# Kernel tuning notes

Hardware: AMD Instinct MI355X
Metric: run time of the kernel (lower is better)

## Reference

```python
import jax, jax.numpy as jnp
import numpy as np

DIM = 512
NSLOTS = 8
ITERS = 3
EPS = 1e-8
LN_EPS = 1e-5
SCALE = DIM ** -0.5


def _ln(x, g, b):
    m = jnp.mean(x, axis=-1, keepdims=True)
    v = jnp.mean((x - m) ** 2, axis=-1, keepdims=True)
    return (x - m) / jnp.sqrt(v + LN_EPS) * g + b


def _gru(x, h, W_ih, W_hh, b_ih, b_hh):
    # PyTorch GRUCell, gate order r,z,n
    gi = x @ W_ih.T + b_ih
    gh = h @ W_hh.T + b_hh
    ir, iz, inn = jnp.split(gi, 3, axis=-1)
    hr, hz, hn = jnp.split(gh, 3, axis=-1)
    r = jax.nn.sigmoid(ir + hr)
    z = jax.nn.sigmoid(iz + hz)
    n = jnp.tanh(inn + r * hn)
    return (1.0 - z) * n + z * h


def _norm_attn(dots):
    # softmax over slot axis, then renormalize over token axis
    a = jax.nn.softmax(dots, axis=1)
    return a / (jnp.sum(a, axis=-1, keepdims=True) + EPS)


def setup_inputs() -> dict:
    key = jax.random.key(0)
    ks = jax.random.split(key, 16)
    b, na, ni = 32, 1024, 3136
    d, hd = DIM, DIM  # hidden_dim = max(dim, 128) = 512
    s = 0.02
    inp = {
        'inputs_audio': jax.random.normal(ks[0], (b, na, d), jnp.float32),
        'inputs_image': jax.random.normal(ks[1], (b, ni, d), jnp.float32),
        'slots_noise': jax.random.normal(ks[2], (b, NSLOTS, d), jnp.float32),
        'slots_mu': jax.random.normal(ks[3], (1, 1, d), jnp.float32),
        'slots_logsigma': jnp.zeros((1, 1, d), jnp.float32),
        'ln_in_g': jnp.ones((d,), jnp.float32), 'ln_in_b': jnp.zeros((d,), jnp.float32),
        'ln_slots_g': jnp.ones((d,), jnp.float32), 'ln_slots_b': jnp.zeros((d,), jnp.float32),
        'ln_ff_g': jnp.ones((d,), jnp.float32), 'ln_ff_b': jnp.zeros((d,), jnp.float32),
        'Wq': jax.random.normal(ks[4], (d, d), jnp.float32) * s, 'bq': jnp.zeros((d,), jnp.float32),
        'Wk': jax.random.normal(ks[5], (d, d), jnp.float32) * s, 'bk': jnp.zeros((d,), jnp.float32),
        'Wv': jax.random.normal(ks[6], (d, d), jnp.float32) * s, 'bv': jnp.zeros((d,), jnp.float32),
        'W_ih': jax.random.normal(ks[7], (3 * d, d), jnp.float32) * s,
        'W_hh': jax.random.normal(ks[8], (3 * d, d), jnp.float32) * s,
        'b_ih': jnp.zeros((3 * d,), jnp.float32), 'b_hh': jnp.zeros((3 * d,), jnp.float32),
        'W1': jax.random.normal(ks[9], (hd, d), jnp.float32) * s, 'b1': jnp.zeros((hd,), jnp.float32),
        'W2': jax.random.normal(ks[10], (d, hd), jnp.float32) * s, 'b2': jnp.zeros((d,), jnp.float32),
    }
    return inp


def reference(inputs_audio, inputs_image, slots_noise, slots_mu, slots_logsigma,
              ln_in_g, ln_in_b, ln_slots_g, ln_slots_b, ln_ff_g, ln_ff_b,
              Wq, bq, Wk, bk, Wv, bv, W_ih, W_hh, b_ih, b_hh, W1, b1, W2, b2):
    b, na, d = inputs_audio.shape
    slots0 = slots_mu + jnp.exp(slots_logsigma) * slots_noise  # [b, S, d]

    ia = _ln(inputs_audio, ln_in_g, ln_in_b)
    ii = _ln(inputs_image, ln_in_g, ln_in_b)
    k_a = ia @ Wk.T + bk
    v_a = ia @ Wv.T + bv
    k_i = ii @ Wk.T + bk
    v_i = ii @ Wv.T + bv

    def mlp(x):
        return jax.nn.relu(x @ W1.T + b1) @ W2.T + b2

    def step(slots, k, v):
        prev = slots
        sn = _ln(slots, ln_slots_g, ln_slots_b)
        q = sn @ Wq.T + bq
        dots = jnp.einsum('bid,bjd->bij', q, k) * SCALE
        attn = _norm_attn(dots)
        upd = jnp.einsum('bjd,bij->bid', v, attn)
        h = _gru(upd.reshape(-1, d), prev.reshape(-1, d), W_ih, W_hh, b_ih, b_hh)
        slots = h.reshape(b, -1, d)
        slots = slots + mlp(_ln(slots, ln_ff_g, ln_ff_b))
        return slots, q, attn

    slots_a, slots_i = slots0, slots0
    for _ in range(ITERS):
        slots_a, q_a, attn_a = step(slots_a, k_a, v_a)
        slots_i, q_i, attn_i = step(slots_i, k_i, v_i)

    cross_ai = _norm_attn(jnp.einsum('bid,bjd->bij', q_a, k_i) * SCALE)  # audio->image
    cross_ia = _norm_attn(jnp.einsum('bid,bjd->bij', q_i, k_a) * SCALE)  # image->audio

    return (slots_a, q_a, k_a, attn_a, cross_ia,
            slots_i, q_i, k_i, attn_i, cross_ai)
```

## Files before the change

### kernel.cpp

```cpp
#include <hip/hip_runtime.h>
#include <hip/hip_bf16.h>

#define DIM 512
#define EPS 1e-8f
#define LN_EPS 1e-5f
#define SCALE 0.04419417382415922f

typedef float f32x4 __attribute__((ext_vector_type(4)));
typedef __bf16 bf16;
typedef __bf16 bf16x8 __attribute__((ext_vector_type(8)));

typedef const __attribute__((address_space(1))) void gvoid;
typedef __attribute__((address_space(3))) void lvoid;

__device__ inline float bf2f_lo(unsigned u) { union { unsigned x; float f; } c; c.x = u << 16; return c.f; }
__device__ inline float bf2f_hi(unsigned u) { union { unsigned x; float f; } c; c.x = u & 0xffff0000u; return c.f; }

#define SBAR() do { __builtin_amdgcn_sched_barrier(0); \
                    __builtin_amdgcn_s_barrier(); \
                    __builtin_amdgcn_sched_barrier(0); } while (0)

__global__ __launch_bounds__(256) void k_stats_convert(
    const float* __restrict__ x, bf16* __restrict__ xbf,
    float* __restrict__ stats, int M)
{
  int row = blockIdx.x * 4 + (threadIdx.x >> 6);
  int lane = threadIdx.x & 63;
  if (row >= M) return;
  const float* xr = x + (size_t)row * DIM;
  float4 a = *(const float4*)(xr + lane * 8);
  float4 b = *(const float4*)(xr + lane * 8 + 4);
  float s  = a.x + a.y + a.z + a.w + b.x + b.y + b.z + b.w;
  float ss = a.x*a.x + a.y*a.y + a.z*a.z + a.w*a.w
           + b.x*b.x + b.y*b.y + b.z*b.z + b.w*b.w;
  for (int off = 32; off; off >>= 1) { s += __shfl_xor(s, off); ss += __shfl_xor(ss, off); }
  float mean = s * (1.0f / DIM);
  float var  = ss * (1.0f / DIM) - mean * mean;
  float rs   = rsqrtf(var + LN_EPS);
  if (lane == 0) { stats[row * 2] = mean; stats[row * 2 + 1] = rs; }
  union { bf16 h[8]; uint4 u; } cv;
  cv.h[0] = (bf16)a.x; cv.h[1] = (bf16)a.y; cv.h[2] = (bf16)a.z; cv.h[3] = (bf16)a.w;
  cv.h[4] = (bf16)b.x; cv.h[5] = (bf16)b.y; cv.h[6] = (bf16)b.z; cv.h[7] = (bf16)b.w;
  *(uint4*)(xbf + (size_t)row * DIM + lane * 8) = cv.u;
}

__global__ __launch_bounds__(256) void k_stats512(
    const float* __restrict__ x, float* __restrict__ stats)
{
  int row = blockIdx.x * 4 + (threadIdx.x >> 6);
  int lane = threadIdx.x & 63;
  const float* xr = x + (size_t)row * DIM;
  float4 a = *(const float4*)(xr + lane * 8);
  float4 b = *(const float4*)(xr + lane * 8 + 4);
  float s  = a.x + a.y + a.z + a.w + b.x + b.y + b.z + b.w;
  float ss = a.x*a.x + a.y*a.y + a.z*a.z + a.w*a.w
           + b.x*b.x + b.y*b.y + b.z*b.z + b.w*b.w;
  for (int off = 32; off; off >>= 1) { s += __shfl_xor(s, off); ss += __shfl_xor(ss, off); }
  float mean = s * (1.0f / DIM);
  float rs   = rsqrtf(ss * (1.0f / DIM) - mean * mean + LN_EPS);
  if (lane == 0) { stats[row * 2] = mean; stats[row * 2 + 1] = rs; }
}

__global__ __launch_bounds__(64) void k_prep(
    const float* __restrict__ Wk, const float* __restrict__ bk,
    const float* __restrict__ Wv, const float* __restrict__ bv,
    const float* __restrict__ g_in, const float* __restrict__ b_in,
    const float* __restrict__ Wq, const float* __restrict__ bq,
    const float* __restrict__ g_s, const float* __restrict__ b_s,
    const float* __restrict__ W1, const float* __restrict__ b1,
    const float* __restrict__ g_f, const float* __restrict__ b_f,
    bf16* __restrict__ wbf, float* __restrict__ c1kv, float* __restrict__ c2kv,
    float* __restrict__ Wqp, float* __restrict__ cq1, float* __restrict__ cq2,
    float* __restrict__ W1p, float* __restrict__ cf1, float* __restrict__ cf2)
{
  int n = blockIdx.x; int lane = threadIdx.x;
  if (n < 1024) {
    const float* W = (n < DIM) ? (Wk + (size_t)n * DIM) : (Wv + (size_t)(n - DIM) * DIM);
    float bias = (n < DIM) ? bk[n] : bv[n - DIM];
    float s1 = 0.f, s2 = 0.f;
    union { bf16 h[8]; uint4 u; } cv;
#pragma unroll
    for (int j = 0; j < 8; ++j) {
      int d = lane * 8 + j;
      float w = W[d];
      float gw = g_in[d] * w;
      s1 += gw; s2 += b_in[d] * w;
      cv.h[j] = (bf16)gw;
    }
    *(uint4*)(wbf + (size_t)n * DIM + lane * 8) = cv.u;
    for (int off = 32; off; off >>= 1) { s1 += __shfl_xor(s1, off); s2 += __shfl_xor(s2, off); }
    if (lane == 0) { c1kv[n] = s1; c2kv[n] = s2 + bias; }
  } else {
    int m; const float* W; float bias; const float* g; const float* b;
    float* Wp; float* cc1; float* cc2;
    if (n < 1536) { m = n - 1024; W = Wq + (size_t)m * DIM; bias = bq[m]; g = g_s; b = b_s; Wp = Wqp; cc1 = cq1; cc2 = cq2; }
    else          { m = n - 1536; W = W1 + (size_t)m * DIM; bias = b1[m]; g = g_f; b = b_f; Wp = W1p; cc1 = cf1; cc2 = cf2; }
    float s1 = 0.f, s2 = 0.f;
    float arr[8];
#pragma unroll
    for (int j = 0; j < 8; ++j) {
      int d = lane * 8 + j;
      float w = W[d];
      float gw = g[d] * w;
      s1 += gw; s2 += b[d] * w;
      arr[j] = gw;
    }
    *(float4*)(Wp + (size_t)m * DIM + lane * 8)     = make_float4(arr[0], arr[1], arr[2], arr[3]);
    *(float4*)(Wp + (size_t)m * DIM + lane * 8 + 4) = make_float4(arr[4], arr[5], arr[6], arr[7]);
    for (int off = 32; off; off >>= 1) { s1 += __shfl_xor(s1, off); s2 += __shfl_xor(s2, off); }
    if (lane == 0) { cc1[m] = s1; cc2[m] = s2 + bias; }
  }
}

__global__ __launch_bounds__(256, 4) void k_kv_gemm(
    const bf16* __restrict__ xa, const bf16* __restrict__ xi,
    const bf16* __restrict__ wbf,
    const float* __restrict__ sa, const float* __restrict__ si,
    const float* __restrict__ c1, const float* __restrict__ c2,
    float* __restrict__ ka, float* __restrict__ ki,
    bf16* __restrict__ kba, bf16* __restrict__ kbi,
    bf16* __restrict__ va, bf16* __restrict__ vi,
    int nblkA, int nblkTot)
{
  __shared__ bf16 As[2][128 * 32];
  __shared__ bf16 Bs[2][128 * 32];
  const int t = threadIdx.x, wave = t >> 6, lane = t & 63;
  int bid = blockIdx.x;
  int rid = (bid & 7) * (nblkTot >> 3) + (bid >> 3);
  bool isA = rid < nblkA;
  int lrid = isA ? rid : rid - nblkA;
  const bf16* x = isA ? xa : xi;
  const float* stats = isA ? sa : si;
  float* kout = isA ? ka : ki;
  bf16* kbf = isA ? kba : kbi;
  bf16* vbf = isA ? va : vi;
  const int row0 = (lrid >> 3) * 128, col0 = (lrid & 7) * 128;
  f32x4 acc[4][4] = {};

  const int sr  = wave * 16 + (lane >> 2);
  const int sgl = ((lane & 3) ^ ((lane >> 3) & 3)) * 8;
  const bf16* asrc = x   + (size_t)(row0 + sr) * DIM + sgl;
  const bf16* bsrc = wbf + (size_t)(col0 + sr) * DIM + sgl;

  auto stage = [&](int buf, int k0) {
#pragma unroll
    for (int p = 0; p < 2; ++p) {
      __builtin_amdgcn_global_load_lds(
          (gvoid*)(asrc + (size_t)(p * 64) * DIM + k0),
          (lvoid*)((char*)&As[buf][0] + (p * 256 + wave * 64) * 16), 16, 0, 0);
      __builtin_amdgcn_global_load_lds(
          (gvoid*)(bsrc + (size_t)(p * 64) * DIM + k0),
          (lvoid*)((char*)&Bs[buf][0] + (p * 256 + wave * 64) * 16), 16, 0, 0);
    }
  };

  const int l15 = lane & 15, q16 = lane >> 4;
  const int wm = wave >> 1, wn = wave & 1;
  const int gpx = (q16 ^ ((l15 >> 1) & 3)) * 8;

  stage(0, 0);
  stage(1, 32);
  asm volatile("s_waitcnt vmcnt(4)" ::: "memory");
  SBAR();
  int cur = 0;
  for (int ks = 0; ks < 16; ++ks) {
    const bf16* Ab = &As[cur][0];
    const bf16* Bb = &Bs[cur][0];
    bf16x8 ax[4], bw[4];
#pragma unroll
    for (int mi = 0; mi < 4; ++mi)
      ax[mi] = *(const bf16x8*)(Ab + (wm * 64 + mi * 16 + l15) * 32 + gpx);
#pragma unroll
    for (int ni = 0; ni < 4; ++ni)
      bw[ni] = *(const bf16x8*)(Bb + (wn * 64 + ni * 16 + l15) * 32 + gpx);
#pragma unroll
    for (int ni = 0; ni < 4; ++ni)
#pragma unroll
      for (int mi = 0; mi < 4; ++mi)
        acc[ni][mi] = __builtin_amdgcn_mfma_f32_16x16x32_bf16(bw[ni], ax[mi], acc[ni][mi], 0, 0, 0);
    SBAR();
    if (ks < 14) {
      stage(cur, (ks + 2) * 32);
      asm volatile("s_waitcnt vmcnt(4)" ::: "memory");
      SBAR();
    } else if (ks == 14) {
      asm volatile("s_waitcnt vmcnt(0)" ::: "memory");
      SBAR();
    }
    cur ^= 1;
  }

#pragma unroll
  for (int mi = 0; mi < 4; ++mi) {
    int row = row0 + wm * 64 + mi * 16 + l15;
    float2 st = *(const float2*)&stats[row * 2];
    float rs = st.y, rm = st.y * st.x;
#pragma unroll
    for (int ni = 0; ni < 4; ++ni) {
      int col = col0 + wn * 64 + ni * 16 + q16 * 4;
      float4 c1v = *(const float4*)&c1[col];
      float4 c2v = *(const float4*)&c2[col];
      f32x4 a = acc[ni][mi];
      float4 o;
      o.x = rs * a[0] - rm * c1v.x + c2v.x;
      o.y = rs * a[1] - rm * c1v.y + c2v.y;
      o.z = rs * a[2] - rm * c1v.z + c2v.z;
      o.w = rs * a[3] - rm * c1v.w + c2v.w;
      union { bf16 h[4]; uint2 u; } pk;
      pk.h[0] = (bf16)o.x; pk.h[1] = (bf16)o.y; pk.h[2] = (bf16)o.z; pk.h[3] = (bf16)o.w;
      if (col0 < DIM) {
        *(float4*)&kout[(size_t)row * DIM + col] = o;
        if (kbf) *(uint2*)&kbf[(size_t)row * DIM + col] = pk.u;
      } else {
        *(uint2*)&vbf[(size_t)row * DIM + (col - DIM)] = pk.u;
      }
    }
  }
}

__global__ __launch_bounds__(256) void k_f2bf(
    const float* __restrict__ in, bf16* __restrict__ out)
{
  size_t i = ((size_t)blockIdx.x * 256 + threadIdx.x) * 8;
  float4 a = *(const float4*)(in + i);
  float4 b = *(const float4*)(in + i + 4);
  union { bf16 h[8]; uint4 u; } cv;
  cv.h[0] = (bf16)a.x; cv.h[1] = (bf16)a.y; cv.h[2] = (bf16)a.z; cv.h[3] = (bf16)a.w;
  cv.h[4] = (bf16)b.x; cv.h[5] = (bf16)b.y; cv.h[6] = (bf16)b.z; cv.h[7] = (bf16)b.w;
  *(uint4*)(out + i) = cv.u;
}

__global__ __launch_bounds__(256) void k_init_slots(
    const float* __restrict__ noise, const float* __restrict__ mu,
    const float* __restrict__ lsig, float* __restrict__ slots)
{
  int idx = blockIdx.x * 256 + threadIdx.x;
  int d = idx & (DIM - 1);
  float v = mu[d] + expf(lsig[d]) * noise[idx];
  slots[idx] = v;
  slots[131072 + idx] = v;
}

template <int MODE>
__global__ __launch_bounds__(128) void k_sgemm(
    const float* __restrict__ A, const float* __restrict__ B, int N,
    float* __restrict__ C,
    const float* __restrict__ c1a, const float* __restrict__ c2a,
    const float* __restrict__ stats,
    const float* __restrict__ bias, const float* __restrict__ invden,
    const float* __restrict__ R,
    float* __restrict__ outA, float* __restrict__ outI,
    bf16* __restrict__ qbf)
{
  __shared__ float As[32][33];
  __shared__ float Bs[64][33];
  int t = threadIdx.x;
  int m0 = blockIdx.y * 32, n0 = blockIdx.x * 64;
  float acc[4][4] = {};
  for (int k0 = 0; k0 < DIM; k0 += 32) {
    __syncthreads();
#pragma unroll
    for (int p = 0; p < 2; ++p) {
      int idx = p * 128 + t, r = idx >> 3, c4 = (idx & 7) * 4;
      float4 v = *(const float4*)(A + (size_t)(m0 + r) * DIM + k0 + c4);
      As[r][c4] = v.x; As[r][c4 + 1] = v.y; As[r][c4 + 2] = v.z; As[r][c4 + 3] = v.w;
    }
#pragma unroll
    for (int p = 0; p < 4; ++p) {
      int idx = p * 128 + t, r = idx >> 3, c4 = (idx & 7) * 4;
      float4 v = *(const float4*)(B + (size_t)(n0 + r) * DIM + k0 + c4);
      Bs[r][c4] = v.x; Bs[r][c4 + 1] = v.y; Bs[r][c4 + 2] = v.z; Bs[r][c4 + 3] = v.w;
    }
    __syncthreads();
    int tr = t >> 4, tc = t & 15;
#pragma unroll
    for (int k = 0; k < 32; ++k) {
      float a0 = As[tr * 4][k], a1 = As[tr * 4 + 1][k], a2 = As[tr * 4 + 2][k], a3 = As[tr * 4 + 3][k];
      float b0 = Bs[tc * 4][k], b1 = Bs[tc * 4 + 1][k], b2 = Bs[tc * 4 + 2][k], b3 = Bs[tc * 4 + 3][k];
      acc[0][0] += a0 * b0; acc[0][1] += a0 * b1; acc[0][2] += a0 * b2; acc[0][3] += a0 * b3;
      acc[1][0] += a1 * b0; acc[1][1] += a1 * b1; acc[1][2] += a1 * b2; acc[1][3] += a1 * b3;
      acc[2][0] += a2 * b0; acc[2][1] += a2 * b1; acc[2][2] += a2 * b2; acc[2][3] += a2 * b3;
      acc[3][0] += a3 * b0; acc[3][1] += a3 * b1; acc[3][2] += a3 * b2; acc[3][3] += a3 * b3;
    }
  }
  int tr = t >> 4, tc = t & 15;
#pragma unroll
  for (int mi = 0; mi < 4; ++mi) {
    int row = m0 + tr * 4 + mi;
#pragma unroll
    for (int ni = 0; ni < 4; ++ni) {
      int col = n0 + tc * 4 + ni;
      float v = acc[mi][ni];
      if (MODE == 0 || MODE == 3) {
        float mean = stats[row * 2], rs = stats[row * 2 + 1];
        v = rs * v - rs * mean * c1a[col] + c2a[col];
      }
      if (MODE == 4) v += bias[col];
      if (MODE == 3) v = fmaxf(v, 0.0f);
      if (MODE == 4) v += R[(size_t)row * N + col];
      if (MODE == 0) {
        if (row < 256) outA[(size_t)row * DIM + col] = v;
        else           outI[(size_t)(row - 256) * DIM + col] = v;
        qbf[(size_t)row * DIM + col] = (bf16)(v * SCALE);
      } else {
        C[(size_t)row * N + col] = v;
        if (MODE == 4 && outA) {
          if (row < 256) outA[(size_t)row * DIM + col] = v;
          else           outI[(size_t)(row - 256) * DIM + col] = v;
        }
      }
    }
  }
}

__global__ __launch_bounds__(128) void k_gates(
    const float* __restrict__ num, const float* __restrict__ slots,
    const float* __restrict__ Wih, const float* __restrict__ Whh,
    const float* __restrict__ bih, const float* __restrict__ bhh,
    const float* __restrict__ invden,
    float* __restrict__ gib, float* __restrict__ ghb)
{
  bool first = blockIdx.x < 24;
  const float* A = first ? num : slots;
  const float* B = first ? Wih : Whh;
  const float* bias = first ? bih : bhh;
  float* C = first ? gib : ghb;
  int n0 = (first ? blockIdx.x : blockIdx.x - 24) * 64;
  int m0 = blockIdx.y * 32;
  __shared__ float As[32][33];
  __shared__ float Bs[64][33];
  int t = threadIdx.x;
  float acc[4][4] = {};
  for (int k0 = 0; k0 < DIM; k0 += 32) {
    __syncthreads();
#pragma unroll
    for (int p = 0; p < 2; ++p) {
      int idx = p * 128 + t, r = idx >> 3, c4 = (idx & 7) * 4;
      float4 v = *(const float4*)(A + (size_t)(m0 + r) * DIM + k0 + c4);
      As[r][c4] = v.x; As[r][c4 + 1] = v.y; As[r][c4 + 2] = v.z; As[r][c4 + 3] = v.w;
    }
#pragma unroll
    for (int p = 0; p < 4; ++p) {
      int idx = p * 128 + t, r = idx >> 3, c4 = (idx & 7) * 4;
      float4 v = *(const float4*)(B + (size_t)(n0 + r) * DIM + k0 + c4);
      Bs[r][c4] = v.x; Bs[r][c4 + 1] = v.y; Bs[r][c4 + 2] = v.z; Bs[r][c4 + 3] = v.w;
    }
    __syncthreads();
    int tr = t >> 4, tc = t & 15;
#pragma unroll
    for (int k = 0; k < 32; ++k) {
      float a0 = As[tr * 4][k], a1 = As[tr * 4 + 1][k], a2 = As[tr * 4 + 2][k], a3 = As[tr * 4 + 3][k];
      float b0 = Bs[tc * 4][k], b1 = Bs[tc * 4 + 1][k], b2 = Bs[tc * 4 + 2][k], b3 = Bs[tc * 4 + 3][k];
      acc[0][0] += a0 * b0; acc[0][1] += a0 * b1; acc[0][2] += a0 * b2; acc[0][3] += a0 * b3;
      acc[1][0] += a1 * b0; acc[1][1] += a1 * b1; acc[1][2] += a1 * b2; acc[1][3] += a1 * b3;
      acc[2][0] += a2 * b0; acc[2][1] += a2 * b1; acc[2][2] += a2 * b2; acc[2][3] += a2 * b3;
      acc[3][0] += a3 * b0; acc[3][1] += a3 * b1; acc[3][2] += a3 * b2; acc[3][3] += a3 * b3;
    }
  }
  int tr = t >> 4, tc = t & 15;
#pragma unroll
  for (int mi = 0; mi < 4; ++mi) {
    int row = m0 + tr * 4 + mi;
    float sc = first ? invden[row] : 1.0f;
#pragma unroll
    for (int ni = 0; ni < 4; ++ni) {
      int col = n0 + tc * 4 + ni;
      C[(size_t)row * 1536 + col] = acc[mi][ni] * sc + bias[col];
    }
  }
}

__global__ __launch_bounds__(256) void k_dots(
    const bf16* __restrict__ qA, const bf16* __restrict__ qI,
    const bf16* __restrict__ kA, const bf16* __restrict__ kI,
    float* __restrict__ aoutA, float* __restrict__ aoutI,
    float* __restrict__ denp, int NA_, int NI_)
{
  __shared__ bf16 ks[2][128 * 64];
  __shared__ float dsh[32];
  int t = threadIdx.x, wave = t >> 6, lane = t & 63;
  int b = blockIdx.y, tile = blockIdx.x;
  bool isA = tile < 8;
  int til = isA ? tile : tile - 8;
  int N = isA ? NA_ : NI_;
  int j0 = til * 128;
  const bf16* q = (isA ? qA : qI) + (size_t)b * 8 * DIM;
  const bf16* k = (isA ? kA : kI) + (size_t)b * N * DIM;
  float* aout = (isA ? aoutA : aoutI) + (size_t)b * 8 * N;
  int drow = (isA ? 0 : 256) + b * 8;

  const int l15 = lane & 15, q16 = lane >> 4;
  bf16x8 afq[16];
  {
    const bf16* qr = q + (size_t)(l15 & 7) * DIM + q16 * 8;
#pragma unroll
    for (int f = 0; f < 16; ++f)
      afq[f] = *(const bf16x8*)(qr + f * 32);
  }

  const int sr  = wave * 8 + (lane >> 3);
  const int sgl = ((lane & 7) ^ (lane >> 3)) * 8;
  int jr = j0 + sr; if (jr > N - 1) jr = N - 1;
  const bf16* ksrc = k + (size_t)jr * DIM + sgl;
  int jr2 = j0 + 32 + sr; if (jr2 > N - 1) jr2 = N - 1;
  const bf16* ksrc2 = k + (size_t)jr2 * DIM + sgl;
  int jr3 = j0 + 64 + sr; if (jr3 > N - 1) jr3 = N - 1;
  const bf16* ksrc3 = k + (size_t)jr3 * DIM + sgl;
  int jr4 = j0 + 96 + sr; if (jr4 > N - 1) jr4 = N - 1;
  const bf16* ksrc4 = k + (size_t)jr4 * DIM + sgl;

  auto stage = [&](int buf, int c) {
    __builtin_amdgcn_global_load_lds((gvoid*)(ksrc  + c * 64),
        (lvoid*)((char*)&ks[buf][0] + (0 * 256 + wave * 64) * 16), 16, 0, 0);
    __builtin_amdgcn_global_load_lds((gvoid*)(ksrc2 + c * 64),
        (lvoid*)((char*)&ks[buf][0] + (1 * 256 + wave * 64) * 16), 16, 0, 0);
    __builtin_amdgcn_global_load_lds((gvoid*)(ksrc3 + c * 64),
        (lvoid*)((char*)&ks[buf][0] + (2 * 256 + wave * 64) * 16), 16, 0, 0);
    __builtin_amdgcn_global_load_lds((gvoid*)(ksrc4 + c * 64),
        (lvoid*)((char*)&ks[buf][0] + (3 * 256 + wave * 64) * 16), 16, 0, 0);
  };

  stage(0, 0);
  stage(1, 1);
  asm volatile("s_waitcnt vmcnt(4)" ::: "memory");
  SBAR();
  f32x4 acc[2] = {};
  int cur = 0;
  for (int c = 0; c < 8; ++c) {
#pragma unroll
    for (int kk = 0; kk < 2; ++kk) {
#pragma unroll
      for (int n = 0; n < 2; ++n) {
        int R = wave * 32 + n * 16 + l15;
        int gp = (kk * 4 + q16) ^ (R & 7);
        bf16x8 bfr = *(const bf16x8*)(&ks[cur][0] + R * 64 + gp * 8);
        acc[n] = __builtin_amdgcn_mfma_f32_16x16x32_bf16(afq[c * 2 + kk], bfr, acc[n], 0, 0, 0);
      }
    }
    SBAR();
    if (c < 6) {
      stage(cur, c + 2);
      asm volatile("s_waitcnt vmcnt(4)" ::: "memory");
      SBAR();
    } else if (c == 6) {
      asm volatile("s_waitcnt vmcnt(0)" ::: "memory");
      SBAR();
    }
    cur ^= 1;
  }

  float dsum[8];
#pragma unroll
  for (int i = 0; i < 8; ++i) dsum[i] = 0.f;
#pragma unroll
  for (int n = 0; n < 2; ++n) {
    int j = j0 + wave * 32 + n * 16 + l15;
    float dv[8];
#pragma unroll
    for (int r = 0; r < 4; ++r) {
      float own = acc[n][r];
      float oth = __shfl_xor(own, 16);
      if (q16 == 0) { dv[r] = own; dv[4 + r] = oth; }
      else          { dv[r] = oth; dv[4 + r] = own; }
    }
    float mx = dv[0];
#pragma unroll
    for (int i = 1; i < 8; ++i) mx = fmaxf(mx, dv[i]);
    float sum = 0.f;
#pragma unroll
    for (int i = 0; i < 8; ++i) { dv[i] = __expf(dv[i] - mx); sum += dv[i]; }
    float inv = 1.0f / sum;
    bool valid = (j < N);
#pragma unroll
    for (int i = 0; i < 8; ++i) {
      float av = valid ? dv[i] * inv : 0.0f;
      dsum[i] += av;
      if (valid && q16 == 0) aout[(size_t)i * N + j] = av;
    }
  }
#pragma unroll
  for (int i = 0; i < 8; ++i) {
    float v = dsum[i];
    v += __shfl_xor(v, 1); v += __shfl_xor(v, 2);
    v += __shfl_xor(v, 4); v += __shfl_xor(v, 8);
    dsum[i] = v;
  }
  if (lane == 0) {
#pragma unroll
    for (int i = 0; i < 8; ++i) dsh[wave * 8 + i] = dsum[i];
  }
  __syncthreads();
  if (t < 8) {
    float den = dsh[t] + dsh[8 + t] + dsh[16 + t] + dsh[24 + t];
    denp[((size_t)drow + t) * 32 + til] = den;
  }
}

__global__ __launch_bounds__(256) void k_upd(
    const bf16* __restrict__ vA, const bf16* __restrict__ vI,
    const float* __restrict__ aA, const float* __restrict__ aI,
    float* __restrict__ numpA, float* __restrict__ numpI, int NA_, int NI_)
{
  __shared__ float ash[128 * 12];
  int t = threadIdx.x, b = blockIdx.y, x = blockIdx.x;
  bool isA = x < 4;
  int c = isA ? x : x - 4;
  int N = isA ? NA_ : NI_;
  int nc = isA ? 4 : 13;
  int jstart = c * 256;
  int jend = jstart + 256; if (jend > N) jend = N;
  const bf16* v = (isA ? vA : vI) + (size_t)b * N * DIM;
  const float* a = (isA ? aA : aI) + (size_t)b * 8 * N;
  float acc[16] = {};
  int d0 = t * 2;
  for (int jt = jstart; jt < jend; jt += 128) {
    int jmax = jend - jt; if (jmax > 128) jmax = 128;
    __syncthreads();
    {
      int i = t >> 5, jq = (t & 31) * 4;
      float4 av = make_float4(0.f, 0.f, 0.f, 0.f);
      if (jt + jq < N) av = *(const float4*)&a[(size_t)i * N + jt + jq];
      ash[(jq + 0) * 12 + i] = av.x;
      ash[(jq + 1) * 12 + i] = av.y;
      ash[(jq + 2) * 12 + i] = av.z;
      ash[(jq + 3) * 12 + i] = av.w;
    }
    __syncthreads();
    for (int jj = 0; jj < jmax; ++jj) {
      unsigned vv = *(const unsigned*)(v + (size_t)(jt + jj) * DIM + d0);
      float v0 = bf2f_lo(vv), v1 = bf2f_hi(vv);
      float4 a0 = *(const float4*)&ash[jj * 12];
      float4 a1 = *(const float4*)&ash[jj * 12 + 4];
      acc[0]  += a0.x * v0; acc[1]  += a0.x * v1;
      acc[2]  += a0.y * v0; acc[3]  += a0.y * v1;
      acc[4]  += a0.z * v0; acc[5]  += a0.z * v1;
      acc[6]  += a0.w * v0; acc[7]  += a0.w * v1;
      acc[8]  += a1.x * v0; acc[9]  += a1.x * v1;
      acc[10] += a1.y * v0; acc[11] += a1.y * v1;
      acc[12] += a1.z * v0; acc[13] += a1.z * v1;
      acc[14] += a1.w * v0; acc[15] += a1.w * v1;
    }
  }
  float* np = (isA ? numpA : numpI) + (((size_t)b * nc + c) * 8) * DIM;
#pragma unroll
  for (int i = 0; i < 8; ++i)
    *(float2*)&np[(size_t)i * DIM + d0] = make_float2(acc[i * 2], acc[i * 2 + 1]);
}

__global__ __launch_bounds__(256) void k_numred(
    const float* __restrict__ numpA, const float* __restrict__ numpI,
    const float* __restrict__ denp,
    float* __restrict__ num, float* __restrict__ invden)
{
  int m = blockIdx.x, t = threadIdx.x;
  bool isA = m < 256;
  int mm = isA ? m : m - 256;
  int bb = mm >> 3, i = mm & 7;
  int nc = isA ? 4 : 13;
  const float* np = (isA ? numpA : numpI) + (((size_t)bb * nc) * 8 + i) * DIM;
  int d0 = t * 2;
  float s0 = 0.f, s1 = 0.f;
  for (int c = 0; c < nc; ++c) {
    float2 vv = *(const float2*)&np[(size_t)c * 8 * DIM + d0];
    s0 += vv.x; s1 += vv.y;
  }
  *(float2*)&num[(size_t)m * DIM + d0] = make_float2(s0, s1);
  if (t == 0) {
    int nch = isA ? 8 : 25;
    float den = EPS;
    for (int c2 = 0; c2 < nch; ++c2) den += denp[(size_t)m * 32 + c2];
    invden[m] = 1.0f / den;
  }
}

__global__ __launch_bounds__(256) void k_gru(
    const float* __restrict__ gi, const float* __restrict__ gh,
    const float* __restrict__ prev,
    float* __restrict__ hout, float* __restrict__ stats_h)
{
  int m = blockIdx.x; int t = threadIdx.x;
  size_t b3 = (size_t)m * 1536, b1 = (size_t)m * DIM;
  float h[2]; float s = 0.f, ss = 0.f;
#pragma unroll
  for (int p = 0; p < 2; ++p) {
    int d = t + p * 256;
    float ir = gi[b3 + d], iz = gi[b3 + 512 + d], in_ = gi[b3 + 1024 + d];
    float hr = gh[b3 + d], hz = gh[b3 + 512 + d], hn = gh[b3 + 1024 + d];
    float r = 1.f / (1.f + __expf(-(ir + hr)));
    float z = 1.f / (1.f + __expf(-(iz + hz)));
    float n = tanhf(in_ + r * hn);
    float hv = (1.f - z) * n + z * prev[b1 + d];
    hout[b1 + d] = hv;
    h[p] = hv; s += hv; ss += hv * hv;
  }
  for (int off = 32; off; off >>= 1) { s += __shfl_xor(s, off); ss += __shfl_xor(ss, off); }
  __shared__ float red[8];
  int wv = t >> 6, ln = t & 63;
  if (ln == 0) { red[wv] = s; red[4 + wv] = ss; }
  __syncthreads();
  s = red[0] + red[1] + red[2] + red[3];
  ss = red[4] + red[5] + red[6] + red[7];
  float mean = s * (1.0f / DIM);
  float rs = rsqrtf(ss * (1.0f / DIM) - mean * mean + LN_EPS);
  if (t == 0) { stats_h[m * 2] = mean; stats_h[m * 2 + 1] = rs; }
}

__global__ __launch_bounds__(256) void k_renorm2(
    const float* __restrict__ aA, const float* __restrict__ aI,
    const float* __restrict__ denp,
    float* __restrict__ outA, float* __restrict__ outI, int NA_, int NI_)
{
  int m = blockIdx.x; int t = threadIdx.x;
  bool isA = m < 256;
  int mm = isA ? m : m - 256;
  int N = isA ? NA_ : NI_;
  int nch = isA ? 8 : 25;
  const float* in = (isA ? aA : aI) + (size_t)mm * N;
  float* out = (isA ? outA : outI) + (size_t)mm * N;
  float den = EPS;
  for (int c = 0; c < nch; ++c) den += denp[(size_t)m * 32 + c];
  float inv = 1.0f / den;
  for (int idx = t; idx * 4 < N; idx += 256) {
    float4 v = *(const float4*)&in[idx * 4];
    v.x *= inv; v.y *= inv; v.z *= inv; v.w *= inv;
    *(float4*)&out[idx * 4] = v;
  }
}

extern "C" void kernel_launch(void* const* d_in, const int* in_sizes, int n_in,
                              void* d_out, int out_size, void* d_ws, size_t ws_size,
                              hipStream_t stream)
{
  (void)in_sizes; (void)n_in; (void)out_size;
  const float* x_a   = (const float*)d_in[0];
  const float* x_i   = (const float*)d_in[1];
  const float* noise = (const float*)d_in[2];
  const float* mu    = (const float*)d_in[3];
  const float* lsig  = (const float*)d_in[4];
  const float* ln_in_g = (const float*)d_in[5];
  const float* ln_in_b = (const float*)d_in[6];
  const float* ln_s_g  = (const float*)d_in[7];
  const float* ln_s_b  = (const float*)d_in[8];
  const float* ln_f_g  = (const float*)d_in[9];
  const float* ln_f_b  = (const float*)d_in[10];
  const float* Wq = (const float*)d_in[11]; const float* bq = (const float*)d_in[12];
  const float* Wk = (const float*)d_in[13]; const float* bk = (const float*)d_in[14];
  const float* Wv = (const float*)d_in[15]; const float* bv = (const float*)d_in[16];
  const float* W_ih = (const float*)d_in[17]; const float* W_hh = (const float*)d_in[18];
  const float* b_ih = (const float*)d_in[19]; const float* b_hh = (const float*)d_in[20];
  const float* W1 = (const float*)d_in[21]; const float* b1 = (const float*)d_in[22];
  const float* W2 = (const float*)d_in[23]; const float* b2 = (const float*)d_in[24];

  const int NA = 1024, NI = 3136;
  const int MA = 32 * NA, MI = 32 * NI;

  float* out = (float*)d_out;
  float* o_slots_a  = out;
  float* o_q_a      = out + 131072;
  float* o_k_a      = out + 262144;
  float* o_attn_a   = out + 17039360;
  float* o_cross_ia = out + 17301504;
  float* o_slots_i  = out + 17563648;
  float* o_q_i      = out + 17694720;
  float* o_k_i      = out + 17825792;
  float* o_attn_i   = out + 69206016;
  float* o_cross_ai = out + 70008832;

  char* w = (char*)d_ws;
  size_t used = 0;
  auto alloc = [&](size_t bytes) {
    char* p = w + used;
    used += (bytes + 255) & ~(size_t)255;
    return p;
  };
  bf16* xbf_a = (bf16*)alloc((size_t)MA * DIM * 2);
  bf16* xbf_i = (bf16*)alloc((size_t)MI * DIM * 2);
  bf16* vbf_a = (bf16*)alloc((size_t)MA * DIM * 2);
  bf16* vbf_i = (bf16*)alloc((size_t)MI * DIM * 2);
  float* stats_a = (float*)alloc((size_t)MA * 2 * 4);
  float* stats_i = (float*)alloc((size_t)MI * 2 * 4);
  bf16* wbf  = (bf16*)alloc(1024 * 512 * 2);
  float* c1kv = (float*)alloc(1024 * 4);
  float* c2kv = (float*)alloc(1024 * 4);
  float* Wqp = (float*)alloc(512 * 512 * 4);
  float* cq1 = (float*)alloc(512 * 4);
  float* cq2 = (float*)alloc(512 * 4);
  float* W1p = (float*)alloc(512 * 512 * 4);
  float* cf1 = (float*)alloc(512 * 4);
  float* cf2 = (float*)alloc(512 * 4);
  float* slots = (float*)alloc(512 * 512 * 4);
  bf16*  qbf   = (bf16*)alloc(512 * 512 * 2);
  float* mid   = (float*)alloc(512 * 512 * 4);
  float* hid   = (float*)alloc(512 * 512 * 4);
  float* num   = (float*)alloc(512 * 512 * 4);
  float* gib   = (float*)alloc(512 * 1536 * 4);
  float* ghb   = (float*)alloc(512 * 1536 * 4);
  float* stats_s = (float*)alloc(512 * 2 * 4);
  float* stats_h = (float*)alloc(512 * 2 * 4);
  float* invden  = (float*)alloc(512 * 4);
  float* denp    = (float*)alloc(512 * 32 * 4);
  float* abuf_a  = (float*)alloc((size_t)256 * NA * 4);
  float* abuf_i  = (float*)alloc((size_t)256 * NI * 4);
  float* numpA   = (float*)alloc((size_t)32 * 4 * 8 * DIM * 4);
  float* numpI   = (float*)alloc((size_t)32 * 13 * 8 * DIM * 4);
  if (used > ws_size) return;

  size_t kbf_bytes = (((size_t)MA * DIM * 2 + 255) & ~(size_t)255)
                   + (((size_t)MI * DIM * 2 + 255) & ~(size_t)255);
  bf16* kbf_a; bf16* kbf_i; bool kbf_fused;
  if (used + kbf_bytes <= ws_size) {
    kbf_a = (bf16*)alloc((size_t)MA * DIM * 2);
    kbf_i = (bf16*)alloc((size_t)MI * DIM * 2);
    kbf_fused = true;
  } else {
    kbf_a = xbf_a; kbf_i = xbf_i;
    kbf_fused = false;
  }

  k_stats_convert<<<MA / 4, 256, 0, stream>>>(x_a, xbf_a, stats_a, MA);
  k_stats_convert<<<MI / 4, 256, 0, stream>>>(x_i, xbf_i, stats_i, MI);
  k_prep<<<2048, 64, 0, stream>>>(Wk, bk, Wv, bv, ln_in_g, ln_in_b,
                                  Wq, bq, ln_s_g, ln_s_b, W1, b1, ln_f_g, ln_f_b,
                                  wbf, c1kv, c2kv, Wqp, cq1, cq2, W1p, cf1, cf2);
  {
    int nblkA = (MA / 128) * 8;
    int nblkTot = nblkA + (MI / 128) * 8;
    k_kv_gemm<<<nblkTot, 256, 0, stream>>>(xbf_a, xbf_i, wbf, stats_a, stats_i,
        c1kv, c2kv, o_k_a, o_k_i,
        kbf_fused ? kbf_a : nullptr, kbf_fused ? kbf_i : nullptr,
        vbf_a, vbf_i, nblkA, nblkTot);
  }
  if (!kbf_fused) {
    k_f2bf<<<MA * DIM / 2048, 256, 0, stream>>>(o_k_a, kbf_a);
    k_f2bf<<<MI * DIM / 2048, 256, 0, stream>>>(o_k_i, kbf_i);
  }
  k_init_slots<<<512, 256, 0, stream>>>(noise, mu, lsig, slots);
  k_stats512<<<128, 256, 0, stream>>>(slots, stats_s);

  for (int it = 0; it < 3; ++it) {
    bool last = (it == 2);
    k_sgemm<0><<<dim3(8, 16), 128, 0, stream>>>(slots, Wqp, DIM, nullptr,
        cq1, cq2, stats_s, nullptr, nullptr, nullptr, o_q_a, o_q_i, qbf);
    k_dots<<<dim3(33, 32), 256, 0, stream>>>(qbf, qbf + 256 * DIM,
        kbf_a, kbf_i, abuf_a, abuf_i, denp, NA, NI);
    k_upd<<<dim3(17, 32), 256, 0, stream>>>(vbf_a, vbf_i, abuf_a, abuf_i, numpA, numpI, NA, NI);
    k_numred<<<512, 256, 0, stream>>>(numpA, numpI, denp, num, invden);
    k_gates<<<dim3(48, 16), 128, 0, stream>>>(num, slots, W_ih, W_hh,
        b_ih, b_hh, invden, gib, ghb);
    k_gru<<<512, 256, 0, stream>>>(gib, ghb, slots, mid, stats_h);
    k_sgemm<3><<<dim3(8, 16), 128, 0, stream>>>(mid, W1p, DIM, hid,
        cf1, cf2, stats_h, nullptr, nullptr, nullptr, nullptr, nullptr, nullptr);
    k_sgemm<4><<<dim3(8, 16), 128, 0, stream>>>(hid, W2, DIM, slots,
        nullptr, nullptr, nullptr, b2, nullptr, mid,
        last ? o_slots_a : nullptr, last ? o_slots_i : nullptr, nullptr);
    if (!last) k_stats512<<<128, 256, 0, stream>>>(slots, stats_s);
  }

  k_renorm2<<<512, 256, 0, stream>>>(abuf_a, abuf_i, denp, o_attn_a, o_attn_i, NA, NI);

  k_dots<<<dim3(33, 32), 256, 0, stream>>>(qbf + 256 * DIM, qbf,
      kbf_a, kbf_i, abuf_a, abuf_i, denp, NA, NI);
  k_renorm2<<<512, 256, 0, stream>>>(abuf_a, abuf_i, denp, o_cross_ia, o_cross_ai, NA, NI);
}
```

Before: 1.111 ms.

## Triple-buffer GEMM and dots pipelines, merge stats launches, fuse slot init stats

The KV GEMM and dots kernels go from double to triple-buffered LDS staging, so loads are issued one step further ahead, and MFMA sections are raised in priority with s_setprio. The two stats_convert launches become a single launch covering both modalities. Slot initialization now computes the LayerNorm stats itself, which removes a separate stats kernel. Raising LDS use lowers the occupancy bound from 4 to 3 blocks, which could offset the deeper prefetch.

```diff
diff --git a/kernel.cpp b/kernel.cpp
--- a/kernel.cpp
+++ b/kernel.cpp
@@ -21,13 +21,17 @@
                     __builtin_amdgcn_sched_barrier(0); } while (0)
 
 __global__ __launch_bounds__(256) void k_stats_convert(
-    const float* __restrict__ x, bf16* __restrict__ xbf,
-    float* __restrict__ stats, int M)
+    const float* __restrict__ xa, const float* __restrict__ xi,
+    bf16* __restrict__ xbfa, bf16* __restrict__ xbfi,
+    float* __restrict__ sa, float* __restrict__ si, int MA)
 {
   int row = blockIdx.x * 4 + (threadIdx.x >> 6);
   int lane = threadIdx.x & 63;
-  if (row >= M) return;
-  const float* xr = x + (size_t)row * DIM;
+  bool isA = row < MA;
+  int lrow = isA ? row : row - MA;
+  const float* xr = (isA ? xa : xi) + (size_t)lrow * DIM;
+  bf16* xbf = (isA ? xbfa : xbfi) + (size_t)lrow * DIM;
+  float* stats = (isA ? sa : si) + (size_t)lrow * 2;
   float4 a = *(const float4*)(xr + lane * 8);
   float4 b = *(const float4*)(xr + lane * 8 + 4);
   float s  = a.x + a.y + a.z + a.w + b.x + b.y + b.z + b.w;
@@ -37,11 +41,11 @@
   float mean = s * (1.0f / DIM);
   float var  = ss * (1.0f / DIM) - mean * mean;
   float rs   = rsqrtf(var + LN_EPS);
-  if (lane == 0) { stats[row * 2] = mean; stats[row * 2 + 1] = rs; }
+  if (lane == 0) { stats[0] = mean; stats[1] = rs; }
   union { bf16 h[8]; uint4 u; } cv;
   cv.h[0] = (bf16)a.x; cv.h[1] = (bf16)a.y; cv.h[2] = (bf16)a.z; cv.h[3] = (bf16)a.w;
   cv.h[4] = (bf16)b.x; cv.h[5] = (bf16)b.y; cv.h[6] = (bf16)b.z; cv.h[7] = (bf16)b.w;
-  *(uint4*)(xbf + (size_t)row * DIM + lane * 8) = cv.u;
+  *(uint4*)(xbf + lane * 8) = cv.u;
 }
 
 __global__ __launch_bounds__(256) void k_stats512(
@@ -112,7 +116,7 @@
   }
 }
 
-__global__ __launch_bounds__(256, 4) void k_kv_gemm(
+__global__ __launch_bounds__(256, 3) void k_kv_gemm(
     const bf16* __restrict__ xa, const bf16* __restrict__ xi,
     const bf16* __restrict__ wbf,
     const float* __restrict__ sa, const float* __restrict__ si,
@@ -122,8 +126,8 @@
     bf16* __restrict__ va, bf16* __restrict__ vi,
     int nblkA, int nblkTot)
 {
-  __shared__ bf16 As[2][128 * 32];
-  __shared__ bf16 Bs[2][128 * 32];
+  __shared__ bf16 As[3][128 * 32];
+  __shared__ bf16 Bs[3][128 * 32];
   const int t = threadIdx.x, wave = t >> 6, lane = t & 63;
   int bid = blockIdx.x;
   int rid = (bid & 7) * (nblkTot >> 3) + (bid >> 3);
@@ -147,10 +151,10 @@
     for (int p = 0; p < 2; ++p) {
       __builtin_amdgcn_global_load_lds(
           (gvoid*)(asrc + (size_t)(p * 64) * DIM + k0),
-          (lvoid*)((char*)&As[buf][0] + (p * 256 + wave * 64) * 16), 16, 0, 0);
+          (lvoid*)((char*)&As[0][0] + buf * 8192 + (p * 256 + wave * 64) * 16), 16, 0, 0);
       __builtin_amdgcn_global_load_lds(
           (gvoid*)(bsrc + (size_t)(p * 64) * DIM + k0),
-          (lvoid*)((char*)&Bs[buf][0] + (p * 256 + wave * 64) * 16), 16, 0, 0);
+          (lvoid*)((char*)&Bs[0][0] + buf * 8192 + (p * 256 + wave * 64) * 16), 16, 0, 0);
     }
   };
 
@@ -160,12 +164,13 @@
 
   stage(0, 0);
   stage(1, 32);
-  asm volatile("s_waitcnt vmcnt(4)" ::: "memory");
+  stage(2, 64);
+  asm volatile("s_waitcnt vmcnt(8)" ::: "memory");
   SBAR();
   int cur = 0;
   for (int ks = 0; ks < 16; ++ks) {
-    const bf16* Ab = &As[cur][0];
-    const bf16* Bb = &Bs[cur][0];
+    const bf16* Ab = &As[0][0] + cur * (128 * 32);
+    const bf16* Bb = &Bs[0][0] + cur * (128 * 32);
     bf16x8 ax[4], bw[4];
 #pragma unroll
     for (int mi = 0; mi < 4; ++mi)
@@ -173,21 +178,25 @@
 #pragma unroll
     for (int ni = 0; ni < 4; ++ni)
       bw[ni] = *(const bf16x8*)(Bb + (wn * 64 + ni * 16 + l15) * 32 + gpx);
+    __builtin_amdgcn_s_setprio(1);
 #pragma unroll
     for (int ni = 0; ni < 4; ++ni)
 #pragma unroll
       for (int mi = 0; mi < 4; ++mi)
         acc[ni][mi] = __builtin_amdgcn_mfma_f32_16x16x32_bf16(bw[ni], ax[mi], acc[ni][mi], 0, 0, 0);
+    __builtin_amdgcn_s_setprio(0);
+    if (ks == 15) break;
     SBAR();
-    if (ks < 14) {
-      stage(cur, (ks + 2) * 32);
+    if (ks < 13) {
+      stage(cur, (ks + 3) * 32);
+      asm volatile("s_waitcnt vmcnt(8)" ::: "memory");
+    } else if (ks == 13) {
       asm volatile("s_waitcnt vmcnt(4)" ::: "memory");
-      SBAR();
-    } else if (ks == 14) {
+    } else {
       asm volatile("s_waitcnt vmcnt(0)" ::: "memory");
-      SBAR();
-    }
-    cur ^= 1;
+    }
+    SBAR();
+    cur = (cur == 2) ? 0 : cur + 1;
   }
 
 #pragma unroll
@@ -232,13 +241,32 @@
 
 __global__ __launch_bounds__(256) void k_init_slots(
     const float* __restrict__ noise, const float* __restrict__ mu,
-    const float* __restrict__ lsig, float* __restrict__ slots)
-{
-  int idx = blockIdx.x * 256 + threadIdx.x;
-  int d = idx & (DIM - 1);
-  float v = mu[d] + expf(lsig[d]) * noise[idx];
-  slots[idx] = v;
-  slots[131072 + idx] = v;
+    const float* __restrict__ lsig, float* __restrict__ slots,
+    float* __restrict__ stats)
+{
+  int row = blockIdx.x;
+  int t = threadIdx.x;
+  int d1 = t + 256;
+  float v0 = mu[t]  + expf(lsig[t])  * noise[row * DIM + t];
+  float v1 = mu[d1] + expf(lsig[d1]) * noise[row * DIM + d1];
+  slots[(size_t)row * DIM + t]  = v0;
+  slots[(size_t)row * DIM + d1] = v1;
+  slots[131072 + (size_t)row * DIM + t]  = v0;
+  slots[131072 + (size_t)row * DIM + d1] = v1;
+  float s = v0 + v1, ss = v0 * v0 + v1 * v1;
+  for (int off = 32; off; off >>= 1) { s += __shfl_xor(s, off); ss += __shfl_xor(ss, off); }
+  __shared__ float red[8];
+  int wv = t >> 6, ln = t & 63;
+  if (ln == 0) { red[wv] = s; red[4 + wv] = ss; }
+  __syncthreads();
+  if (t == 0) {
+    s = red[0] + red[1] + red[2] + red[3];
+    ss = red[4] + red[5] + red[6] + red[7];
+    float mean = s * (1.0f / DIM);
+    float rs = rsqrtf(ss * (1.0f / DIM) - mean * mean + LN_EPS);
+    stats[row * 2] = mean; stats[row * 2 + 1] = rs;
+    stats[(row + 256) * 2] = mean; stats[(row + 256) * 2 + 1] = rs;
+  }
 }
 
 template <int MODE>
@@ -370,13 +398,13 @@
   }
 }
 
-__global__ __launch_bounds__(256) void k_dots(
+__global__ __launch_bounds__(256, 3) void k_dots(
     const bf16* __restrict__ qA, const bf16* __restrict__ qI,
     const bf16* __restrict__ kA, const bf16* __restrict__ kI,
     float* __restrict__ aoutA, float* __restrict__ aoutI,
     float* __restrict__ denp, int NA_, int NI_)
 {
-  __shared__ bf16 ks[2][128 * 64];
+  __shared__ bf16 ks[3][128 * 64];
   __shared__ float dsh[32];
   int t = threadIdx.x, wave = t >> 6, lane = t & 63;
   int b = blockIdx.y, tile = blockIdx.x;
@@ -411,42 +439,48 @@
 
   auto stage = [&](int buf, int c) {
     __builtin_amdgcn_global_load_lds((gvoid*)(ksrc  + c * 64),
-        (lvoid*)((char*)&ks[buf][0] + (0 * 256 + wave * 64) * 16), 16, 0, 0);
+        (lvoid*)((char*)&ks[0][0] + buf * 16384 + (0 * 256 + wave * 64) * 16), 16, 0, 0);
     __builtin_amdgcn_global_load_lds((gvoid*)(ksrc2 + c * 64),
-        (lvoid*)((char*)&ks[buf][0] + (1 * 256 + wave * 64) * 16), 16, 0, 0);
+        (lvoid*)((char*)&ks[0][0] + buf * 16384 + (1 * 256 + wave * 64) * 16), 16, 0, 0);
     __builtin_amdgcn_global_load_lds((gvoid*)(ksrc3 + c * 64),
-        (lvoid*)((char*)&ks[buf][0] + (2 * 256 + wave * 64) * 16), 16, 0, 0);
+        (lvoid*)((char*)&ks[0][0] + buf * 16384 + (2 * 256 + wave * 64) * 16), 16, 0, 0);
     __builtin_amdgcn_global_load_lds((gvoid*)(ksrc4 + c * 64),
-        (lvoid*)((char*)&ks[buf][0] + (3 * 256 + wave * 64) * 16), 16, 0, 0);
+        (lvoid*)((char*)&ks[0][0] + buf * 16384 + (3 * 256 + wave * 64) * 16), 16, 0, 0);
   };
 
   stage(0, 0);
   stage(1, 1);
-  asm volatile("s_waitcnt vmcnt(4)" ::: "memory");
+  stage(2, 2);
+  asm volatile("s_waitcnt vmcnt(8)" ::: "memory");
   SBAR();
   f32x4 acc[2] = {};
   int cur = 0;
   for (int c = 0; c < 8; ++c) {
+    const bf16* kb = &ks[0][0] + cur * (128 * 64);
+    __builtin_amdgcn_s_setprio(1);
 #pragma unroll
     for (int kk = 0; kk < 2; ++kk) {
 #pragma unroll
       for (int n = 0; n < 2; ++n) {
         int R = wave * 32 + n * 16 + l15;
         int gp = (kk * 4 + q16) ^ (R & 7);
-        bf16x8 bfr = *(const bf16x8*)(&ks[cur][0] + R * 64 + gp * 8);
+        bf16x8 bfr = *(const bf16x8*)(kb + R * 64 + gp * 8);
         acc[n] = __builtin_amdgcn_mfma_f32_16x16x32_bf16(afq[c * 2 + kk], bfr, acc[n], 0, 0, 0);
       }
     }
+    __builtin_amdgcn_s_setprio(0);
+    if (c == 7) break;
     SBAR();
-    if (c < 6) {
-      stage(cur, c + 2);
+    if (c < 5) {
+      stage(cur, c + 3);
+      asm volatile("s_waitcnt vmcnt(8)" ::: "memory");
+    } else if (c == 5) {
       asm volatile("s_waitcnt vmcnt(4)" ::: "memory");
-      SBAR();
-    } else if (c == 6) {
+    } else {
       asm volatile("s_waitcnt vmcnt(0)" ::: "memory");
-      SBAR();
-    }
-    cur ^= 1;
+    }
+    SBAR();
+    cur = (cur == 2) ? 0 : cur + 1;
   }
 
   float dsum[8];
@@ -717,8 +751,8 @@
     kbf_fused = false;
   }
 
-  k_stats_convert<<<MA / 4, 256, 0, stream>>>(x_a, xbf_a, stats_a, MA);
-  k_stats_convert<<<MI / 4, 256, 0, stream>>>(x_i, xbf_i, stats_i, MI);
+  k_stats_convert<<<(MA + MI) / 4, 256, 0, stream>>>(x_a, x_i, xbf_a, xbf_i,
+                                                     stats_a, stats_i, MA);
   k_prep<<<2048, 64, 0, stream>>>(Wk, bk, Wv, bv, ln_in_g, ln_in_b,
                                   Wq, bq, ln_s_g, ln_s_b, W1, b1, ln_f_g, ln_f_b,
                                   wbf, c1kv, c2kv, Wqp, cq1, cq2, W1p, cf1, cf2);
@@ -734,8 +768,7 @@
     k_f2bf<<<MA * DIM / 2048, 256, 0, stream>>>(o_k_a, kbf_a);
     k_f2bf<<<MI * DIM / 2048, 256, 0, stream>>>(o_k_i, kbf_i);
   }
-  k_init_slots<<<512, 256, 0, stream>>>(noise, mu, lsig, slots);
-  k_stats512<<<128, 256, 0, stream>>>(slots, stats_s);
+  k_init_slots<<<256, 256, 0, stream>>>(noise, mu, lsig, slots, stats_s);
 
   for (int it = 0; it < 3; ++it) {
     bool last = (it == 2);
```

Result: no change. 1.121 ms (+0.9%).
